# Performance work log

Hardware: AMD Instinct MI355X
Metric: run time of the kernel (lower is better)

Reference implementation:

```python
import jax, jax.numpy as jnp
import numpy as np

H = 12          # num attention heads
D = 768         # hidden size
DH = D // H     # head dim = 64

def setup_inputs() -> dict:
    key = jax.random.key(0)
    ks = jax.random.split(key, 9)
    B, N = 8, 1024
    s = 0.02
    return {
        "hidden_states": jax.random.normal(ks[0], (B, N, D), jnp.float32),
        "Wq": jax.random.normal(ks[1], (D, D), jnp.float32) * s,
        "bq": jnp.zeros((D,), jnp.float32),
        "Wk": jax.random.normal(ks[2], (D, D), jnp.float32) * s,
        "bk": jnp.zeros((D,), jnp.float32),
        "Wv": jax.random.normal(ks[3], (D, D), jnp.float32) * s,
        "bv": jnp.zeros((D,), jnp.float32),
        "Wo": jax.random.normal(ks[4], (D, D), jnp.float32) * s,
        "bo": jnp.zeros((D,), jnp.float32),
    }

def _split_heads(x):
    # [B, N, D] -> [B, H, N, DH]
    B, N, _ = x.shape
    return x.reshape(B, N, H, DH).transpose(0, 2, 1, 3)

def reference(hidden_states, Wq, bq, Wk, bk, Wv, bv, Wo, bo):
    # torch Linear: y = x @ W.T + b
    q = _split_heads(hidden_states @ Wq.T + bq)
    k = _split_heads(hidden_states @ Wk.T + bk)
    v = _split_heads(hidden_states @ Wv.T + bv)
    scale = 1.0 / jnp.sqrt(jnp.asarray(DH, hidden_states.dtype))
    scores = jnp.einsum("bhqd,bhkd->bhqk", q, k) * scale
    probs = jax.nn.softmax(scores, axis=-1)
    ctx = jnp.einsum("bhqk,bhkd->bhqd", probs, v)
    B, _, N, _ = ctx.shape
    ctx = ctx.transpose(0, 2, 1, 3).reshape(B, N, D)
    return ctx @ Wo.T + bo
```

## Files before the change

### kernel.cpp

```cpp
#include <hip/hip_runtime.h>

typedef unsigned short u16;
typedef unsigned int   u32;
typedef unsigned long long u64;
typedef __attribute__((ext_vector_type(8))) short bf16x8;
typedef __attribute__((ext_vector_type(4))) float f32x4;
typedef __attribute__((address_space(3))) u32 lds_u32;
typedef __attribute__((address_space(1))) u32 gbl_u32;

#define MFMA16(a,b,c) __builtin_amdgcn_mfma_f32_16x16x32_bf16((a),(b),(c),0,0,0)
#define QSCALE 0.1803368801111204f

#define WAIT8 do{ asm volatile("s_waitcnt vmcnt(8)" ::: "memory"); }while(0)
#define WAIT4 do{ asm volatile("s_waitcnt vmcnt(4)" ::: "memory"); }while(0)
#define WAIT0 do{ asm volatile("s_waitcnt vmcnt(0)" ::: "memory"); }while(0)
#define SCHED __builtin_amdgcn_sched_barrier(0)
#define BARR  __builtin_amdgcn_s_barrier()

__device__ __forceinline__ u16 f2bf(float f){
  u32 u = __builtin_bit_cast(u32, f);
  u32 r = u + 0x7fffu + ((u>>16)&1u);
  return (u16)(r>>16);
}
__device__ __forceinline__ float bf2f(u16 h){
  return __builtin_bit_cast(float, (u32)h<<16);
}

union V8 { u16 s[8]; uint4 v; };

__global__ __launch_bounds__(256) void cvt_all(const float* __restrict__ hs,
    const float* __restrict__ Wq, const float* __restrict__ Wk,
    const float* __restrict__ Wv, const float* __restrict__ Wo,
    u16* __restrict__ hsb, u16* __restrict__ wqkv, u16* __restrict__ woh)
{
  const int bid = blockIdx.x;
  if (bid < 3072){
    int i = bid*256 + threadIdx.x;
    const float4* p = (const float4*)(hs + (size_t)i*8);
    float4 a = p[0], b = p[1];
    V8 t;
    t.s[0]=f2bf(a.x); t.s[1]=f2bf(a.y); t.s[2]=f2bf(a.z); t.s[3]=f2bf(a.w);
    t.s[4]=f2bf(b.x); t.s[5]=f2bf(b.y); t.s[6]=f2bf(b.z); t.s[7]=f2bf(b.w);
    *(uint4*)(hsb + (size_t)i*8) = t.v;
    return;
  }
  const int r = bid - 3072;
  const int seg = r / 288;
  const int off = (r - seg*288)*256 + threadIdx.x;
  const float* src = seg==0?Wq: seg==1?Wk: seg==2?Wv: Wo;
  const float4* p = (const float4*)(src + (size_t)off*8);
  float4 a = p[0], b = p[1];
  float xs[8] = {a.x,a.y,a.z,a.w,b.x,b.y,b.z,b.w};
  V8 t;
  #pragma unroll
  for (int j=0;j<8;++j) t.s[j]=f2bf(xs[j]);
  if (seg < 3) *(uint4*)(wqkv + (size_t)seg*589824 + (size_t)off*8) = t.v;
  else         *(uint4*)(woh  + (size_t)off*8) = t.v;
}

__global__ __launch_bounds__(256) void mm_qkv(const u16* __restrict__ A, const u16* __restrict__ Bp,
    const float* __restrict__ bq, const float* __restrict__ bk, const float* __restrict__ bvv,
    u16* __restrict__ Oq, u16* __restrict__ Ok, u16* __restrict__ Ov)
{
  __shared__ u16 P[4][8192];
  const int bid = blockIdx.x;
  const int sid = (bid & 7)*144 + (bid >> 3);
  const int mb = sid/18, nb = sid - mb*18;
  const int m0 = mb*128, n0 = nb*128;
  const int tid = threadIdx.x;
  const int lane = tid&63, wid = tid>>6;
  const int wr = wid>>1, wc = wid&1;
  const int fr = lane&15, fg = lane>>4;

  const char* Ab = (const char*)A;
  const char* Bb = (const char*)Bp;
  const char* sp[4];
  #pragma unroll
  for (int c=0;c<4;++c){
    int ci = c*256 + tid;
    int row = ci>>3, slot = ci&7;
    int d = slot ^ (row&7);
    if (d < 4) sp[c] = Ab + (size_t)(m0+row)*1536 + d*16;
    else       sp[c] = Bb + (size_t)(n0+row)*1536 + (d-4)*16;
  }
  const int sA = (fg ^ (fr&7)) << 4;
  const int sB = sA ^ 64;

  f32x4 zz = {0.f,0.f,0.f,0.f};
  f32x4 acc[4][4];
  #pragma unroll
  for (int i=0;i<4;++i)
    #pragma unroll
    for (int j=0;j<4;++j) acc[i][j]=zz;

  auto STAGE = [&](int t){
    char* dst0 = (char*)P[t&3];
    #pragma unroll
    for (int c=0;c<4;++c)
      __builtin_amdgcn_global_load_lds((const gbl_u32*)(sp[c] + (size_t)t*64),
        (lds_u32*)(dst0 + c*4096 + wid*1024), 16, 0, 0);
  };
  auto COMPUTE = [&](int t){
    const char* pb = (const char*)P[t&3];
    bf16x8 bfr[4];
    #pragma unroll
    for (int nt=0;nt<4;++nt)
      bfr[nt] = *(const bf16x8*)(pb + (wc*64+nt*16+fr)*128 + sB);
    #pragma unroll
    for (int mt=0;mt<4;++mt){
      bf16x8 af = *(const bf16x8*)(pb + (wr*64+mt*16+fr)*128 + sA);
      #pragma unroll
      for (int nt=0;nt<4;++nt)
        acc[mt][nt] = MFMA16(af, bfr[nt], acc[mt][nt]);
    }
  };

  STAGE(0); STAGE(1); STAGE(2);
  for (int t=0; t<24; ++t){
    if (t < 22) WAIT8; else if (t == 22) WAIT4; else WAIT0;
    SCHED; BARR; SCHED;
    if (t < 21) STAGE(t+3);
    __builtin_amdgcn_s_setprio(1);
    COMPUTE(t);
    __builtin_amdgcn_s_setprio(0);
    SCHED; BARR;
  }

  const int seg = nb/6;
  const float* bias = seg==0?bq: seg==1?bk:bvv;
  const float sc = (seg==0) ? QSCALE : 1.0f;
  if (seg < 2){
    u16* O = seg==0?Oq:Ok;
    #pragma unroll
    for (int mt=0;mt<4;++mt){
      #pragma unroll
      for (int nt=0;nt<4;++nt){
        int colw = n0 + wc*64 + nt*16 + fr - seg*768;
        float bz = bias[colw];
        int hh = colw>>6, d = colw&63;
        #pragma unroll
        for (int rr=0;rr<4;++rr){
          int row = m0 + wr*64 + mt*16 + fg*4 + rr;
          int b = row>>10, nn = row&1023;
          O[((size_t)(b*12+hh)<<16) + (size_t)nn*64 + d] = f2bf((acc[mt][nt][rr] + bz) * sc);
        }
      }
    }
  } else {
    #pragma unroll
    for (int mt=0;mt<4;++mt){
      #pragma unroll
      for (int nt=0;nt<4;++nt){
        int colw = n0 + wc*64 + nt*16 + fr - 1536;
        float bz = bias[colw];
        int hh = colw>>6, d = colw&63;
        int row0 = m0 + wr*64 + mt*16 + fg*4;
        int b = row0>>10, nn = row0&1023;
        union { u16 h[4]; u64 q; } pk;
        #pragma unroll
        for (int rr=0;rr<4;++rr) pk.h[rr] = f2bf(acc[mt][nt][rr] + bz);
        *(u64*)&Ov[((size_t)(b*12+hh)<<16) + (size_t)d*1024 + nn] = pk.q;
      }
    }
  }
}

__global__ __launch_bounds__(256) void mm_o(const u16* __restrict__ A, const u16* __restrict__ Bp,
                                            const float* __restrict__ bias, float* __restrict__ O)
{
  __shared__ u16 P[4][8192];
  const int bid = blockIdx.x;
  const int sid = (bid & 7)*48 + (bid >> 3);
  const int mb = sid/6, nb = sid - mb*6;
  const int m0 = mb*128, n0 = nb*128;
  const int tid = threadIdx.x;
  const int lane = tid&63, wid = tid>>6;
  const int wr = wid>>1, wc = wid&1;
  const int fr = lane&15, fg = lane>>4;

  const char* Ab = (const char*)A;
  const char* Bb = (const char*)Bp;
  const char* sp[4];
  #pragma unroll
  for (int c=0;c<4;++c){
    int ci = c*256 + tid;
    int row = ci>>3, slot = ci&7;
    int d = slot ^ (row&7);
    if (d < 4) sp[c] = Ab + (size_t)(m0+row)*1536 + d*16;
    else       sp[c] = Bb + (size_t)(n0+row)*1536 + (d-4)*16;
  }
  const int sA = (fg ^ (fr&7)) << 4;
  const int sB = sA ^ 64;

  f32x4 zz = {0.f,0.f,0.f,0.f};
  f32x4 acc[4][4];
  #pragma unroll
  for (int i=0;i<4;++i)
    #pragma unroll
    for (int j=0;j<4;++j) acc[i][j]=zz;

  auto STAGE = [&](int t){
    char* dst0 = (char*)P[t&3];
    #pragma unroll
    for (int c=0;c<4;++c)
      __builtin_amdgcn_global_load_lds((const gbl_u32*)(sp[c] + (size_t)t*64),
        (lds_u32*)(dst0 + c*4096 + wid*1024), 16, 0, 0);
  };
  auto COMPUTE = [&](int t){
    const char* pb = (const char*)P[t&3];
    bf16x8 bfr[4];
    #pragma unroll
    for (int nt=0;nt<4;++nt)
      bfr[nt] = *(const bf16x8*)(pb + (wc*64+nt*16+fr)*128 + sB);
    #pragma unroll
    for (int mt=0;mt<4;++mt){
      bf16x8 af = *(const bf16x8*)(pb + (wr*64+mt*16+fr)*128 + sA);
      #pragma unroll
      for (int nt=0;nt<4;++nt)
        acc[mt][nt] = MFMA16(af, bfr[nt], acc[mt][nt]);
    }
  };

  STAGE(0); STAGE(1); STAGE(2);
  for (int t=0; t<24; ++t){
    if (t < 22) WAIT8; else if (t == 22) WAIT4; else WAIT0;
    SCHED; BARR; SCHED;
    if (t < 21) STAGE(t+3);
    __builtin_amdgcn_s_setprio(1);
    COMPUTE(t);
    __builtin_amdgcn_s_setprio(0);
    SCHED; BARR;
  }

  #pragma unroll
  for (int mt=0;mt<4;++mt){
    #pragma unroll
    for (int nt=0;nt<4;++nt){
      int colb = n0 + wc*64 + nt*16 + fr;
      float bz = bias[colb];
      #pragma unroll
      for (int rr=0;rr<4;++rr){
        int row = m0 + wr*64 + mt*16 + fg*4 + rr;
        O[(size_t)row*768 + colb] = acc[mt][nt][rr] + bz;
      }
    }
  }
}

__global__ __launch_bounds__(256) void attn(const u16* __restrict__ qh, const u16* __restrict__ kh,
                                            const u16* __restrict__ vh, u16* __restrict__ ch)
{
  __shared__ u16 Kb[2][4096];
  __shared__ u16 Vb[2][4096];
  __shared__ u16 Ps[4][32][72];
  const int tid=threadIdx.x, w=tid>>6, lane=tid&63;
  const int fr=lane&15, fg=lane>>4;
  const int bh=blockIdx.x, qt=blockIdx.y;
  const size_t base=(size_t)bh<<16;
  const int q0=qt*128 + w*32;

  const char* kbase = (const char*)(kh + base);
  const char* vbase = (const char*)(vh + base);

  int koff[2], voff[2];
  #pragma unroll
  for (int c=0;c<2;++c){
    int ci = c*256 + tid;
    int row = ci>>3;
    int colp = ((ci&7)*16) ^ ((row&7)<<4);
    koff[c] = row*128  + colp;
    voff[c] = row*2048 + colp;
  }

  bf16x8 qf[2][2];
  #pragma unroll
  for (int mt=0;mt<2;++mt)
    #pragma unroll
    for (int ks=0;ks<2;++ks)
      qf[mt][ks] = *(const bf16x8*)&qh[base + (size_t)(q0+mt*16+fr)*64 + ks*32 + fg*8];

  const int swz = (fr&7)<<4;
  int lowD[2];
  #pragma unroll
  for (int ks=0;ks<2;++ks) lowD[ks] = (ks*64 + fg*16) ^ swz;
  const int frbase = fr*128;

  f32x4 zz = {0.f,0.f,0.f,0.f};
  f32x4 o[2][4];
  float lr[2][4];
  #pragma unroll
  for (int mt=0;mt<2;++mt)
    #pragma unroll
    for (int j=0;j<4;++j){ o[mt][j]=zz; lr[mt][j]=0.f; }

  {
    #pragma unroll
    for (int c=0;c<2;++c){
      __builtin_amdgcn_global_load_lds((const gbl_u32*)(kbase + koff[c]),
        (lds_u32*)((char*)&Kb[0][0] + c*4096 + w*1024), 16, 0, 0);
      __builtin_amdgcn_global_load_lds((const gbl_u32*)(vbase + voff[c]),
        (lds_u32*)((char*)&Vb[0][0] + c*4096 + w*1024), 16, 0, 0);
    }
  }
  __syncthreads();

  for (int kt=0; kt<16; ++kt){
    const int buf = kt & 1;
    {
      const int ktn = (kt+1) & 15;
      const char* kt_ = kbase + ktn*8192;
      const char* vt_ = vbase + ktn*128;
      #pragma unroll
      for (int c=0;c<2;++c){
        __builtin_amdgcn_global_load_lds((const gbl_u32*)(kt_ + koff[c]),
          (lds_u32*)((char*)&Kb[buf^1][0] + c*4096 + w*1024), 16, 0, 0);
        __builtin_amdgcn_global_load_lds((const gbl_u32*)(vt_ + voff[c]),
          (lds_u32*)((char*)&Vb[buf^1][0] + c*4096 + w*1024), 16, 0, 0);
      }
    }

    f32x4 s[2][4];
    #pragma unroll
    for (int mt=0;mt<2;++mt)
      #pragma unroll
      for (int j=0;j<4;++j) s[mt][j]=zz;
    const char* kb = (const char*)&Kb[buf][0];
    __builtin_amdgcn_s_setprio(1);
    #pragma unroll
    for (int ct=0;ct<4;++ct){
      #pragma unroll
      for (int ks=0;ks<2;++ks){
        bf16x8 kf = *(const bf16x8*)(kb + ct*2048 + frbase + lowD[ks]);
        s[0][ct]=MFMA16(qf[0][ks],kf,s[0][ct]);
        s[1][ct]=MFMA16(qf[1][ks],kf,s[1][ct]);
      }
    }
    __builtin_amdgcn_s_setprio(0);

    #pragma unroll
    for (int mt=0;mt<2;++mt){
      #pragma unroll
      for (int rr=0;rr<4;++rr){
        int qr = mt*16+fg*4+rr;
        float acc_l = 0.f;
        #pragma unroll
        for (int ct=0;ct<4;++ct){
          float e = __builtin_amdgcn_exp2f(s[mt][ct][rr]);
          u32 u = __builtin_bit_cast(u32, e);
          acc_l += __builtin_bit_cast(float, u & 0xffff0000u);
          Ps[w][qr][ct*16+fr] = (u16)(u>>16);
        }
        lr[mt][rr] += acc_l;
      }
    }

    const char* vb = (const char*)&Vb[buf][0];
    __builtin_amdgcn_s_setprio(1);
    #pragma unroll
    for (int ks2=0;ks2<2;++ks2){
      bf16x8 vf[4];
      #pragma unroll
      for (int dt=0;dt<4;++dt)
        vf[dt] = *(const bf16x8*)(vb + dt*2048 + frbase + lowD[ks2]);
      #pragma unroll
      for (int mt=0;mt<2;++mt){
        bf16x8 pa = *(const bf16x8*)&Ps[w][mt*16+fr][ks2*32+fg*8];
        #pragma unroll
        for (int dt=0;dt<4;++dt)
          o[mt][dt]=MFMA16(pa, vf[dt], o[mt][dt]);
      }
    }
    __builtin_amdgcn_s_setprio(0);

    __syncthreads();
  }

  float inv[2][4];
  #pragma unroll
  for (int mt=0;mt<2;++mt)
    #pragma unroll
    for (int rr=0;rr<4;++rr){
      float l = lr[mt][rr];
      l += __shfl_xor(l,1); l += __shfl_xor(l,2);
      l += __shfl_xor(l,4); l += __shfl_xor(l,8);
      inv[mt][rr] = 1.0f / l;
    }
  const int b=bh/12, hd=bh%12;
  #pragma unroll
  for (int mt=0;mt<2;++mt){
    #pragma unroll
    for (int dt=0;dt<4;++dt){
      int d = dt*16 + fr;
      #pragma unroll
      for (int rr=0;rr<4;++rr){
        int n = q0 + mt*16 + fg*4 + rr;
        ch[((size_t)b*1024 + n)*768 + hd*64 + d] = f2bf(o[mt][dt][rr] * inv[mt][rr]);
      }
    }
  }
}

extern "C" void kernel_launch(void* const* d_in, const int* in_sizes, int n_in,
                              void* d_out, int out_size, void* d_ws, size_t ws_size,
                              hipStream_t stream) {
  const float* hs = (const float*)d_in[0];
  const float* Wq = (const float*)d_in[1];
  const float* bq = (const float*)d_in[2];
  const float* Wk = (const float*)d_in[3];
  const float* bk = (const float*)d_in[4];
  const float* Wv = (const float*)d_in[5];
  const float* bv = (const float*)d_in[6];
  const float* Wo = (const float*)d_in[7];
  const float* bo = (const float*)d_in[8];
  float* out = (float*)d_out;

  const size_t PS = (size_t)8192*768;
  u16* ws16  = (u16*)d_ws;
  u16* hs_bf = ws16;
  u16* q_bf  = ws16 + PS;
  u16* k_bf  = ws16 + 2*PS;
  u16* v_bf  = ws16 + 3*PS;
  u16* wqkv  = ws16 + 4*PS;
  u16* woh   = wqkv + 3*589824;
  u16* c_hi  = hs_bf;

  dim3 blk(256);
  cvt_all<<<3072 + 4*288, blk, 0, stream>>>(hs, Wq, Wk, Wv, Wo, hs_bf, wqkv, woh);
  mm_qkv<<<1152, blk, 0, stream>>>(hs_bf, wqkv, bq, bk, bv, q_bf, k_bf, v_bf);
  attn<<<dim3(96,8), blk, 0, stream>>>(q_bf, k_bf, v_bf, c_hi);
  mm_o<<<384, blk, 0, stream>>>(c_hi, woh, bo, out);
}
```

Measured before the change: 122.1 us.

## Use triple-buffered LDS pipeline with one barrier per k-step in GEMMs

Both projection GEMMs go from a 4-deep LDS ring with prefetch distance 3 and two barriers per iteration to a 3-deep ring with prefetch distance 2 and a single barrier per iteration. The smaller ring cuts LDS per block from 64KB to 48KB, which may let more blocks fit per CU, and removing the trailing barrier reduces synchronisation stalls. In exchange, less latency is hidden by the shallower prefetch, and the buffer rotation has to stay race-free with only one barrier.

```diff
diff --git a/kernel.cpp b/kernel.cpp
--- a/kernel.cpp
+++ b/kernel.cpp
@@ -11,7 +11,6 @@
 #define MFMA16(a,b,c) __builtin_amdgcn_mfma_f32_16x16x32_bf16((a),(b),(c),0,0,0)
 #define QSCALE 0.1803368801111204f
 
-#define WAIT8 do{ asm volatile("s_waitcnt vmcnt(8)" ::: "memory"); }while(0)
 #define WAIT4 do{ asm volatile("s_waitcnt vmcnt(4)" ::: "memory"); }while(0)
 #define WAIT0 do{ asm volatile("s_waitcnt vmcnt(0)" ::: "memory"); }while(0)
 #define SCHED __builtin_amdgcn_sched_barrier(0)
@@ -62,7 +61,7 @@
     const float* __restrict__ bq, const float* __restrict__ bk, const float* __restrict__ bvv,
     u16* __restrict__ Oq, u16* __restrict__ Ok, u16* __restrict__ Ov)
 {
-  __shared__ u16 P[4][8192];
+  __shared__ u16 P[3][8192];
   const int bid = blockIdx.x;
   const int sid = (bid & 7)*144 + (bid >> 3);
   const int mb = sid/18, nb = sid - mb*18;
@@ -93,15 +92,15 @@
     #pragma unroll
     for (int j=0;j<4;++j) acc[i][j]=zz;
 
-  auto STAGE = [&](int t){
-    char* dst0 = (char*)P[t&3];
+  auto STAGE = [&](int t, int b){
+    char* dst0 = (char*)P[b];
     #pragma unroll
     for (int c=0;c<4;++c)
       __builtin_amdgcn_global_load_lds((const gbl_u32*)(sp[c] + (size_t)t*64),
         (lds_u32*)(dst0 + c*4096 + wid*1024), 16, 0, 0);
   };
-  auto COMPUTE = [&](int t){
-    const char* pb = (const char*)P[t&3];
+  auto COMPUTE = [&](int b){
+    const char* pb = (const char*)P[b];
     bf16x8 bfr[4];
     #pragma unroll
     for (int nt=0;nt<4;++nt)
@@ -115,15 +114,19 @@
     }
   };
 
-  STAGE(0); STAGE(1); STAGE(2);
+  STAGE(0, 0); STAGE(1, 1);
+  int cb = 0;
   for (int t=0; t<24; ++t){
-    if (t < 22) WAIT8; else if (t == 22) WAIT4; else WAIT0;
-    SCHED; BARR; SCHED;
-    if (t < 21) STAGE(t+3);
+    if (t < 23) WAIT4; else WAIT0;
+    BARR; SCHED;
+    if (t < 22){
+      int sb = cb + 2; if (sb >= 3) sb -= 3;
+      STAGE(t+2, sb);
+    }
     __builtin_amdgcn_s_setprio(1);
-    COMPUTE(t);
+    COMPUTE(cb);
     __builtin_amdgcn_s_setprio(0);
-    SCHED; BARR;
+    cb = (cb == 2) ? 0 : cb + 1;
   }
 
   const int seg = nb/6;
@@ -168,7 +171,7 @@
 __global__ __launch_bounds__(256) void mm_o(const u16* __restrict__ A, const u16* __restrict__ Bp,
                                             const float* __restrict__ bias, float* __restrict__ O)
 {
-  __shared__ u16 P[4][8192];
+  __shared__ u16 P[3][8192];
   const int bid = blockIdx.x;
   const int sid = (bid & 7)*48 + (bid >> 3);
   const int mb = sid/6, nb = sid - mb*6;
@@ -199,15 +202,15 @@
     #pragma unroll
     for (int j=0;j<4;++j) acc[i][j]=zz;
 
-  auto STAGE = [&](int t){
-    char* dst0 = (char*)P[t&3];
+  auto STAGE = [&](int t, int b){
+    char* dst0 = (char*)P[b];
     #pragma unroll
     for (int c=0;c<4;++c)
       __builtin_amdgcn_global_load_lds((const gbl_u32*)(sp[c] + (size_t)t*64),
         (lds_u32*)(dst0 + c*4096 + wid*1024), 16, 0, 0);
   };
-  auto COMPUTE = [&](int t){
-    const char* pb = (const char*)P[t&3];
+  auto COMPUTE = [&](int b){
+    const char* pb = (const char*)P[b];
     bf16x8 bfr[4];
     #pragma unroll
     for (int nt=0;nt<4;++nt)
@@ -221,15 +224,19 @@
     }
   };
 
-  STAGE(0); STAGE(1); STAGE(2);
+  STAGE(0, 0); STAGE(1, 1);
+  int cb = 0;
   for (int t=0; t<24; ++t){
-    if (t < 22) WAIT8; else if (t == 22) WAIT4; else WAIT0;
-    SCHED; BARR; SCHED;
-    if (t < 21) STAGE(t+3);
+    if (t < 23) WAIT4; else WAIT0;
+    BARR; SCHED;
+    if (t < 22){
+      int sb = cb + 2; if (sb >= 3) sb -= 3;
+      STAGE(t+2, sb);
+    }
     __builtin_amdgcn_s_setprio(1);
-    COMPUTE(t);
+    COMPUTE(cb);
     __builtin_amdgcn_s_setprio(0);
-    SCHED; BARR;
+    cb = (cb == 2) ? 0 : cb + 1;
   }
 
   #pragma unroll
```

Measured after the change: 119.5 us. 1.02x faster.
